# Optimization experiments

Hardware: AMD Instinct MI355X
Metric: run time of the kernel (lower is better)

Reference implementation:

```python
import jax, jax.numpy as jnp
import numpy as np

N_PULSES = 64
BATCH = 16384
N_STATES = 21


def setup_inputs() -> dict:
    key = jax.random.key(0)
    k = jax.random.split(key, 6)
    flip_angles = jax.random.uniform(k[0], (N_PULSES,), jnp.float32) * jnp.pi          # 0..pi rad
    phases = jax.random.uniform(k[1], (N_PULSES,), jnp.float32) * 2.0 * jnp.pi         # 0..2pi rad
    T1 = 500.0 + 1000.0 * jax.random.uniform(k[2], (BATCH,), jnp.float32)
    T2 = 50.0 + 100.0 * jax.random.uniform(k[3], (BATCH,), jnp.float32)
    B0 = 50.0 * jax.random.normal(k[4], (BATCH,), jnp.float32)                         # Hz
    B1 = 0.8 + 0.4 * jax.random.uniform(k[5], (BATCH,), jnp.float32)                   # unitless
    return {"flip_angles": flip_angles, "phases": phases, "T1": T1, "T2": T2,
            "B0": B0, "B1": B1, "TR": 500, "TE": 10}


def _epg_forward(flip_angles, phases, T1, T2, B0, B1, TR):
    B = T1.shape[0]
    E1 = jnp.exp(-TR / T1)[:, None]                 # (B,1)
    E2 = jnp.exp(-TR / T2)[:, None]                 # (B,1)
    phi = (2.0 * jnp.pi * B0 * TR / 1000.0)[:, None]
    eb0p = jnp.exp(1j * phi.astype(jnp.complex64))  # (B,1) complex64
    eb0m = jnp.conj(eb0p)
    B1c = B1[:, None]

    Fp0 = jnp.zeros((B, N_STATES), jnp.complex64)
    Fm0 = jnp.zeros((B, N_STATES), jnp.complex64)
    Z0 = jnp.zeros((B, N_STATES), jnp.float32).at[:, 0].set(1.0)

    def step(carry, ab):
        Fp, Fm, Z = carry
        a, b = ab
        # relax
        Fp = E2 * Fp
        Fm = E2 * Fm
        Z = (E1 * Z).at[:, 0].add(1.0 - E1[:, 0])
        # B0 dephasing
        Fp = Fp * eb0p
        Fm = Fm * eb0m
        # RF rotation (B1-scaled flip angle)
        alpha = a * B1c                              # (B,1)
        ca = jnp.cos(alpha / 2)
        sa = jnp.sin(alpha / 2)
        eib = jnp.exp(1j * b.astype(jnp.complex64))  # scalar
        emib = jnp.conj(eib)
        Zc = Z.astype(jnp.complex64)
        Fp_n = ca**2 * Fp + sa**2 * jnp.conj(Fm) * eib**2 + 1j * ca * sa * (Zc * eib)
        Fm_n = sa**2 * jnp.conj(Fp) * emib**2 + ca**2 * Fm - 1j * ca * sa * (Zc * emib)
        Z_n = (-1j * sa * ca * (Fp * emib - Fm * eib) + (ca**2 - sa**2) * Zc).real
        # gradient shift
        Fp_s = jnp.roll(Fp_n, 1, axis=1).at[:, 0].set(0)
        Fm_s = jnp.roll(Fm_n, -1, axis=1).at[:, -1].set(0)
        out = jnp.stack([Fp_s.real, Fp_s.imag, Fm_s.real, Fm_s.imag, Z_n], axis=0)
        return (Fp_s, Fm_s, Z_n), out

    _, outs = jax.lax.scan(step, (Fp0, Fm0, Z0), (flip_angles, phases))
    return outs  # (N, 5, B, S): [Fp.re, Fp.im, Fm.re, Fm.im, Z] per pulse


def reference(flip_angles, phases, T1, T2, B0, B1, TR, TE):
    TRf = jnp.float32(TR)
    return _epg_forward(flip_angles, phases, T1, T2, B0, B1, TRf)
```

## Files before the change

kernel.cpp:

```cpp
#include <hip/hip_runtime.h>

namespace {
constexpr int NP      = 64;
constexpr int BATCH_N = 16384;
constexpr int NS      = 21;
constexpr int CHAN    = BATCH_N * NS;
constexpr long long STEP = 5LL * CHAN;
}

__global__ __launch_bounds__(256) void epg_kernel(
    const float* __restrict__ flip, const float* __restrict__ ph,
    const float* __restrict__ T1,   const float* __restrict__ T2,
    const float* __restrict__ B0,   const float* __restrict__ B1,
    const int*   __restrict__ TRp,  float* __restrict__ out)
{
  const int lane = threadIdx.x & 63;
  const int wv   = threadIdx.x >> 6;
  const int sub  = lane / 21;
  const int s    = lane - sub * 21;
  const int bg   = (blockIdx.x * 4 + wv) * 3 + sub;
  const bool active = (sub < 3) && (bg < BATCH_N);
  const int  bs  = active ? bg : 0;

  const float TR = (float)TRp[0];
  const float E1 = __expf(-TR / T1[bs]);
  const float E2 = __expf(-TR / T2[bs]);
  const float b1 = B1[bs];
  const float rec = (s == 0) ? (1.0f - E1) : 0.0f;
  const float phi = 6.283185307179586f * 0.001f * TR * B0[bs];
  float bi, br; __sincosf(phi, &bi, &br);

  float fpr = 0.f, fpi = 0.f, fmr = 0.f, fmi = 0.f;
  float z = (s == 0) ? 1.0f : 0.0f;

  float* op = out + (long long)bs * NS + s;

  for (int p = 0; p < NP; ++p) {
    const float a = flip[p];
    const float b = ph[p];
    float sa, ca; __sincosf(0.5f * a * b1, &sa, &ca);
    float ei, er; __sincosf(b, &ei, &er);
    const float w2r = er * er - ei * ei;
    const float w2i = 2.0f * er * ei;
    const float c2 = ca * ca, s2 = sa * sa, cs = ca * sa;

    fpr *= E2; fpi *= E2; fmr *= E2; fmi *= E2;
    z = E1 * z + rec;

    {
      float t = fpr * br - fpi * bi;
      fpi = fpr * bi + fpi * br; fpr = t;
      float u = fmr * br + fmi * bi;
      fmi = fmi * br - fmr * bi; fmr = u;
    }

    const float zcs = cs * z;
    const float fpnr =  c2 * fpr + s2 * (fmr * w2r + fmi * w2i) - zcs * ei;
    const float fpni =  c2 * fpi + s2 * (fmr * w2i - fmi * w2r) + zcs * er;
    const float fmnr =  c2 * fmr + s2 * (fpr * w2r - fpi * w2i) - zcs * ei;
    const float fmni =  c2 * fmi - s2 * (fpr * w2i + fpi * w2r) - zcs * er;
    const float zn   =  cs * ((fpi - fmi) * er - (fpr + fmr) * ei)
                        + (c2 - s2) * z;

    const float ufpr = __shfl_up(fpnr, 1);
    const float ufpi = __shfl_up(fpni, 1);
    const float dfmr = __shfl_down(fmnr, 1);
    const float dfmi = __shfl_down(fmni, 1);
    fpr = (s == 0)  ? 0.f : ufpr;
    fpi = (s == 0)  ? 0.f : ufpi;
    fmr = (s == 20) ? 0.f : dfmr;
    fmi = (s == 20) ? 0.f : dfmi;
    z = zn;

    if (active) {
      op[0]        = fpr;
      op[CHAN]     = fpi;
      op[2 * CHAN] = fmr;
      op[3 * CHAN] = fmi;
      op[4 * CHAN] = zn;
    }
    op += STEP;
  }
}

extern "C" void kernel_launch(void* const* d_in, const int* in_sizes, int n_in,
                              void* d_out, int out_size, void* d_ws, size_t ws_size,
                              hipStream_t stream) {
  const float* flip = (const float*)d_in[0];
  const float* ph   = (const float*)d_in[1];
  const float* T1   = (const float*)d_in[2];
  const float* T2   = (const float*)d_in[3];
  const float* B0   = (const float*)d_in[4];
  const float* B1   = (const float*)d_in[5];
  const int*   TR   = (const int*)d_in[6];
  float* out = (float*)d_out;

  const int blocks = (BATCH_N + 11) / 12;
  epg_kernel<<<blocks, 256, 0, stream>>>(flip, ph, T1, T2, B0, B1, TR, out);
}
```

Before: 524.8 us.

## Stage per-pulse outputs in double-buffered LDS and write with float4 stores

Each wave writes its per-pulse Fp/Fm/Z values into a double-buffered shared-memory tile. After a block barrier, threads copy the contiguous 12-batch x 21-state chunk of each channel to global memory with 16-byte vector stores. This replaces scattered 4-byte stores from 63 of 64 lanes with aligned wide stores, and byte offsets are computed in 32-bit unsigned arithmetic. The cost is a __syncthreads per pulse and extra LDS traffic.

```diff
diff --git a/kernel.cpp b/kernel.cpp
--- a/kernel.cpp
+++ b/kernel.cpp
@@ -4,8 +4,12 @@
 constexpr int NP      = 64;
 constexpr int BATCH_N = 16384;
 constexpr int NS      = 21;
+constexpr int BPB     = 12;
 constexpr int CHAN    = BATCH_N * NS;
-constexpr long long STEP = 5LL * CHAN;
+constexpr unsigned CHANB = (unsigned)CHAN * 4u;
+constexpr unsigned STEPB = 5u * CHANB;
+constexpr int LDSF    = BPB * NS * 5;
+constexpr int NSLOT   = (LDSF + 3) / 4;
 }
 
 __global__ __launch_bounds__(256) void epg_kernel(
@@ -14,13 +18,30 @@
     const float* __restrict__ B0,   const float* __restrict__ B1,
     const int*   __restrict__ TRp,  float* __restrict__ out)
 {
-  const int lane = threadIdx.x & 63;
-  const int wv   = threadIdx.x >> 6;
+  __shared__ __align__(16) float lds[2][LDSF];
+
+  const int tid  = threadIdx.x;
+  const int lane = tid & 63;
+  const int wv   = tid >> 6;
   const int sub  = lane / 21;
   const int s    = lane - sub * 21;
-  const int bg   = (blockIdx.x * 4 + wv) * 3 + sub;
+  const int bg   = blockIdx.x * BPB + wv * 3 + sub;
   const bool active = (sub < 3) && (bg < BATCH_N);
   const int  bs  = active ? bg : 0;
+  const int  inner = wv * 63 + lane;
+
+  const int rem = min(BPB, BATCH_N - blockIdx.x * BPB);
+  const unsigned base0 = (unsigned)blockIdx.x * (BPB * NS * 4u);
+  int      loff[2]; unsigned goff[2]; bool fdo[2];
+  #pragma unroll
+  for (int k = 0; k < 2; ++k) {
+    const int i = tid + k * 256;
+    const int c = i / 63;
+    const int j = i - c * 63;
+    fdo[k]  = (i < NSLOT) && (4 * j < rem * NS);
+    loff[k] = c * (BPB * NS) + 4 * j;
+    goff[k] = base0 + (unsigned)c * CHANB + (unsigned)j * 16u;
+  }
 
   const float TR = (float)TRp[0];
   const float E1 = __expf(-TR / T1[bs]);
@@ -33,7 +54,9 @@
   float fpr = 0.f, fpi = 0.f, fmr = 0.f, fmi = 0.f;
   float z = (s == 0) ? 1.0f : 0.0f;
 
-  float* op = out + (long long)bs * NS + s;
+  char* const outb = (char*)out;
+  unsigned pbase = 0;
+  int buf = 0;
 
   for (int p = 0; p < NP; ++p) {
     const float a = flip[p];
@@ -73,13 +96,27 @@
     z = zn;
 
     if (active) {
-      op[0]        = fpr;
-      op[CHAN]     = fpi;
-      op[2 * CHAN] = fmr;
-      op[3 * CHAN] = fmi;
-      op[4 * CHAN] = zn;
+      float* lb = lds[buf];
+      lb[inner]                = fpr;
+      lb[BPB * NS + inner]     = fpi;
+      lb[2 * BPB * NS + inner] = fmr;
+      lb[3 * BPB * NS + inner] = fmi;
+      lb[4 * BPB * NS + inner] = zn;
     }
-    op += STEP;
+    __syncthreads();
+
+    {
+      const float* lb = lds[buf];
+      #pragma unroll
+      for (int k = 0; k < 2; ++k) {
+        if (fdo[k]) {
+          const float4 v = *(const float4*)&lb[loff[k]];
+          *(float4*)(outb + pbase + goff[k]) = v;
+        }
+      }
+    }
+    buf ^= 1;
+    pbase += STEPB;
   }
 }
 
@@ -95,6 +132,6 @@
   const int*   TR   = (const int*)d_in[6];
   float* out = (float*)d_out;
 
-  const int blocks = (BATCH_N + 11) / 12;
+  const int blocks = (BATCH_N + BPB - 1) / BPB;
   epg_kernel<<<blocks, 256, 0, stream>>>(flip, ph, T1, T2, B0, B1, TR, out);
 }
```

New measurement: 518.9 us. Within noise of the previous version (-1.1%).
